# Optimization experiments

Hardware: AMD Instinct MI355X
Metric: run time of the kernel (lower is better)

Reference implementation:

```python
import jax, jax.numpy as jnp
import numpy as np

N_HEADS = 8
NUM_CLASSES = 8
ATTN_INTENSE = 1.0


def setup_inputs() -> dict:
    key = jax.random.key(0)
    k1, k2, k3, k4 = jax.random.split(key, 4)
    bs, width, T = 8, 1536, 1024
    qkv = jax.random.normal(k1, (bs, width, T), dtype=jnp.float32)
    attn_mask = jax.random.randint(k2, (bs, 32, 32), 0, NUM_CLASSES, dtype=jnp.int32)
    # class embedding table: NUM_CLASSES rows + 1 null row (used for the global pass)
    embed_table = jax.random.normal(k3, (NUM_CLASSES + 1, 512), dtype=jnp.float32) * 0.02
    # Conv1d(embed_dim=512 -> 3*ch=192, kernel=1, bias=False) weight
    W_cls = jax.random.normal(k4, (192, 512), dtype=jnp.float32) * 0.02
    return {"qkv": qkv, "attn_mask": attn_mask, "embed_table": embed_table, "W_cls": W_cls}


def _attend(q, k, v, scale):
    # q,k,v: [B, T, C]; returns [B, T, C]
    logits = jnp.einsum('btc,bsc->bts', q * scale, k * scale)
    w = jax.nn.softmax(logits, axis=-1)
    return jnp.einsum('bts,bsc->btc', w, v)


def reference(qkv, attn_mask, embed_table, W_cls):
    bs, width, T = qkv.shape
    H = N_HEADS
    ch = width // (3 * H)            # 64
    scale = ch ** -0.25              # 1/sqrt(sqrt(ch))
    bH = bs * H

    qkv_h = qkv.reshape(bH, 3 * ch, T)
    q = jnp.transpose(qkv_h[:, 0 * ch:1 * ch], (0, 2, 1))  # [bH, T, ch]
    k = jnp.transpose(qkv_h[:, 1 * ch:2 * ch], (0, 2, 1))
    v = jnp.transpose(qkv_h[:, 2 * ch:3 * ch], (0, 2, 1))

    # ---- global pass with null class token ----
    null_tok = W_cls @ embed_table[NUM_CLASSES]  # [3*ch]
    qn, kn, vn = null_tok[:ch], null_tok[ch:2 * ch], null_tok[2 * ch:]
    a = _attend(q + qn, k + kn, v + vn, scale)   # [bH, T, ch]

    # ---- per-region (per segmentation class) attention ----
    seg = attn_mask.reshape(bs, T)
    segs = jnp.repeat(seg, H, axis=0)            # [bH, T], sample-major like qkv reshape

    out = a
    counter = jnp.ones((bH, T), dtype=qkv.dtype)
    for c in range(NUM_CLASSES):
        tok = W_cls @ embed_table[c]             # [3*ch], same token at every region position
        qc, kc, vc = tok[:ch], tok[ch:2 * ch], tok[2 * ch:]
        m = segs == c                            # [bH, T]
        logits = jnp.einsum('btc,bsc->bts', (q + qc) * scale, (k + kc) * scale)
        logits = jnp.where(m[:, None, :], logits, -1e9)   # restrict keys to region
        w = jax.nn.softmax(logits, axis=-1)
        a_c = jnp.einsum('bts,bsc->btc', w, v + vc)
        out = out + jnp.where(m[:, :, None], a_c, 0.0)    # scatter-add onto region queries
        counter = counter + ATTN_INTENSE * m.astype(counter.dtype)

    out = out / counter[:, :, None]              # [bH, T, ch]
    # faithful to original: outs are [ch, T] each, torch.stack(dim=1) -> [ch, bH, T], then reshape
    stacked = jnp.transpose(out, (2, 0, 1))      # [ch, bH, T]
    return stacked.reshape(bs, H * ch, T)
```

## Files before the change

### kernel.cpp

```cpp
#include <hip/hip_runtime.h>
#include <stdint.h>

typedef unsigned short u16;
typedef unsigned int   u32;
typedef __bf16 bf16_t;
typedef bf16_t bf16x8 __attribute__((ext_vector_type(8)));
typedef bf16_t bf16x2 __attribute__((ext_vector_type(2)));
typedef float  f32x2  __attribute__((ext_vector_type(2)));
typedef float  f32x4  __attribute__((ext_vector_type(4)));

#define QSCALE 0.18033688011112042f

__device__ __forceinline__ u32 pkbf(float a, float b) {
  f32x2 x = {a, b};
  bf16x2 y = __builtin_convertvector(x, bf16x2);
  union { bf16x2 v; u32 u; } c; c.v = y; return c.u;
}

__device__ __forceinline__ float fexp2(float x) {
#if __has_builtin(__builtin_amdgcn_exp2f)
  return __builtin_amdgcn_exp2f(x);
#else
  float r;
  asm("v_exp_f32 %0, %1\n\ts_nop 0" : "=v"(r) : "v"(x));
  return r;
#endif
}

__device__ __forceinline__ void gload_lds16(const void* g, void* l) {
  __builtin_amdgcn_global_load_lds(
      (const __attribute__((address_space(1))) void*)g,
      (__attribute__((address_space(3))) void*)l, 16, 0, 0);
}

__global__ __launch_bounds__(256)
void prep_kernel(const float* __restrict__ qkv,
                 const float* __restrict__ W, const float* __restrict__ E,
                 float* __restrict__ tok, u16* __restrict__ tiles) {
  const int B = blockIdx.x;
  const int tid = threadIdx.x;
  if (B >= 1024) {
    const int gw = (B - 1024) * 4 + (tid >> 6);
    const int lane = tid & 63;
    if (gw < 1728) {
      const int c = gw / 192, j = gw - c * 192;
      const f32x4* w4 = (const f32x4*)(W + (size_t)j * 512 + lane * 8);
      const f32x4* e4 = (const f32x4*)(E + (size_t)c * 512 + lane * 8);
      float acc = 0.f;
#pragma unroll
      for (int i = 0; i < 2; ++i) {
        f32x4 w = w4[i], e = e4[i];
        acc += w.x * e.x + w.y * e.y + w.z * e.z + w.w * e.w;
      }
#pragma unroll
      for (int off = 32; off; off >>= 1) acc += __shfl_xor(acc, off, 64);
      if (lane == 0) tok[c * 192 + j] = acc;
    }
    return;
  }
  const int bh = B >> 4, kt = B & 15;
  const int s0 = kt * 64;
  const float* qg = qkv + (size_t)bh * 192 * 1024;
  u16* img = tiles + (size_t)B * 8192;
  {
    const int s = tid & 63, g = tid >> 6;
    const float* kb = qg + (size_t)(64 + g * 16) * 1024 + s0 + s;
    float kf[16];
#pragma unroll
    for (int i = 0; i < 16; ++i) kf[i] = kb[(size_t)i * 1024];
    u32 kp[8];
#pragma unroll
    for (int j2 = 0; j2 < 8; ++j2) kp[j2] = pkbf(kf[2 * j2], kf[2 * j2 + 1]);
    const int xr = (s & 7) << 3;
    *(uint4*)&img[s * 64 + ((g * 16)     ^ xr)] = make_uint4(kp[0], kp[1], kp[2], kp[3]);
    *(uint4*)&img[s * 64 + ((g * 16 + 8) ^ xr)] = make_uint4(kp[4], kp[5], kp[6], kp[7]);
  }
  {
    const int g = tid & 15, dg = tid >> 4;
    const int cp = ((g >> 3) & 1) * 32 + (g & 3) * 8 + ((g >> 2) & 1) * 4;
    const float* vb = qg + (size_t)(128 + dg * 4) * 1024 + s0 + g * 4;
#pragma unroll
    for (int i = 0; i < 4; ++i) {
      f32x4 v = *(const f32x4*)(vb + (size_t)i * 1024);
      const int d = dg * 4 + i;
      *(uint2*)&img[4096 + d * 64 + (cp ^ ((d & 7) << 3))] =
          make_uint2(pkbf(v.x, v.y), pkbf(v.z, v.w));
    }
  }
}

__global__ __launch_bounds__(256, 2)
void attn_kernel(const float* __restrict__ qkv, const int* __restrict__ seg,
                 const float* __restrict__ tok, const u16* __restrict__ tiles,
                 float* __restrict__ out) {
  __shared__ __align__(16) u16 smem[16896];

  const int L  = blockIdx.x;
  const int bh = (L & 7) * 8 + ((L >> 3) & 7);
  const int qb = L >> 6;
  const int b  = bh >> 3;
  const int tid = threadIdx.x, wave = tid >> 6, lane = tid & 63;
  const int quad = lane >> 4, l16 = lane & 15;

  const float* qg   = qkv + (size_t)bh * 192 * 1024;
  const int*   segb = seg + b * 1024;
  const u16*   tbh  = tiles + (size_t)bh * (16 * 8192);

  const int q0i = qb * 128 + wave * 32;
  const int tqA = q0i + l16, tqB = tqA + 16;
  const int mycA = segb[tqA], mycB = segb[tqB];
  int sqA[4], sqB[4];
#pragma unroll
  for (int r = 0; r < 4; ++r) {
    sqA[r] = segb[q0i + quad * 4 + r];
    sqB[r] = segb[q0i + 16 + quad * 4 + r];
  }

  const float* tn  = tok + 8 * 192;
  const float* tcA = tok + mycA * 192;
  const float* tcB = tok + mycB * 192;
  union { u32 w[4]; bf16x8 v; } qA0[2], qAb[2], qB0[2], qBb[2];
#pragma unroll
  for (int kc = 0; kc < 2; ++kc)
#pragma unroll
    for (int jj = 0; jj < 4; ++jj) {
      int d = kc * 32 + quad * 8 + jj * 2;
      float a0 = qg[(size_t)d * 1024 + tqA];
      float a1 = qg[(size_t)(d + 1) * 1024 + tqA];
      float b0 = qg[(size_t)d * 1024 + tqB];
      float b1 = qg[(size_t)(d + 1) * 1024 + tqB];
      qA0[kc].w[jj] = pkbf((a0 + tn[d])  * QSCALE, (a1 + tn[d + 1])  * QSCALE);
      qAb[kc].w[jj] = pkbf((a0 + tcA[d]) * QSCALE, (a1 + tcA[d + 1]) * QSCALE);
      qB0[kc].w[jj] = pkbf((b0 + tn[d])  * QSCALE, (b1 + tn[d + 1])  * QSCALE);
      qBb[kc].w[jj] = pkbf((b0 + tcB[d]) * QSCALE, (b1 + tcB[d + 1]) * QSCALE);
    }

  f32x4 OA0[4], OAb[4], OB0[4], OBb[4];
#pragma unroll
  for (int dt = 0; dt < 4; ++dt) {
    OA0[dt] = (f32x4){0.f, 0.f, 0.f, 0.f};  OAb[dt] = (f32x4){0.f, 0.f, 0.f, 0.f};
    OB0[dt] = (f32x4){0.f, 0.f, 0.f, 0.f};  OBb[dt] = (f32x4){0.f, 0.f, 0.f, 0.f};
  }
  float rsA0 = 0.f, rsAb = 0.f, rsB0 = 0.f, rsBb = 0.f;

  {
    const char* src = (const char*)tbh + tid * 16;
    char* dst = (char*)smem + tid * 16;
#pragma unroll
    for (int i = 0; i < 4; ++i) gload_lds16(src + i * 4096, dst + i * 4096);
  }

  const int xq = (l16 & 7) << 3;

#pragma unroll 2
  for (int kt = 0; kt < 16; ++kt) {
    const int s0 = kt * 64;
    __syncthreads();
    if (kt + 1 < 16) {
      const char* src = (const char*)tbh + (size_t)(kt + 1) * 16384 + tid * 16;
      char* dst = (char*)smem + ((kt + 1) & 1) * 16384 + tid * 16;
#pragma unroll
      for (int i = 0; i < 4; ++i) gload_lds16(src + i * 4096, dst + i * 4096);
    }
    int sk[4][4];
#pragma unroll
    for (int n4 = 0; n4 < 4; ++n4) {
      int4 s4 = *(const int4*)&segb[s0 + n4 * 16 + quad * 4];
      sk[n4][0] = s4.x; sk[n4][1] = s4.y; sk[n4][2] = s4.z; sk[n4][3] = s4.w;
    }

    const u16* ktr = smem + (kt & 1) * 8192;
    const u16* vls = ktr + 4096;

    f32x4 SA0[4], SAb[4], SB0[4], SBb[4];
#pragma unroll
    for (int n4 = 0; n4 < 4; ++n4) {
      const int srow = n4 * 16 + l16;
      f32x4 a0 = {0.f, 0.f, 0.f, 0.f}, ab = {0.f, 0.f, 0.f, 0.f};
      f32x4 c0 = {0.f, 0.f, 0.f, 0.f}, cb = {0.f, 0.f, 0.f, 0.f};
#pragma unroll
      for (int kc = 0; kc < 2; ++kc) {
        bf16x8 kfr = *(const bf16x8*)&ktr[srow * 64 + ((kc * 32 + quad * 8) ^ xq)];
        a0 = __builtin_amdgcn_mfma_f32_16x16x32_bf16(kfr, qA0[kc].v, a0, 0, 0, 0);
        ab = __builtin_amdgcn_mfma_f32_16x16x32_bf16(kfr, qAb[kc].v, ab, 0, 0, 0);
        c0 = __builtin_amdgcn_mfma_f32_16x16x32_bf16(kfr, qB0[kc].v, c0, 0, 0, 0);
        cb = __builtin_amdgcn_mfma_f32_16x16x32_bf16(kfr, qBb[kc].v, cb, 0, 0, 0);
      }
      SA0[n4] = a0; SAb[n4] = ab; SB0[n4] = c0; SBb[n4] = cb;
    }

    union { u32 w[4]; bf16x8 v; } paA0[2], paAb[2], paB0[2], paBb[2];
#define SOFTMAX_PACK(S0, Sb, myc, rs0, rsb, pa0, pab)                          \
    {                                                                          \
      float p0[4][4], pb[4][4];                                                \
      _Pragma("unroll")                                                        \
      for (int n4 = 0; n4 < 4; ++n4)                                           \
        _Pragma("unroll")                                                      \
        for (int r = 0; r < 4; ++r) {                                          \
          p0[n4][r] = fexp2(S0[n4][r]);                                        \
          pb[n4][r] = (sk[n4][r] == myc) ? fexp2(Sb[n4][r]) : 0.f;             \
        }                                                                      \
      _Pragma("unroll")                                                        \
      for (int n4 = 0; n4 < 4; ++n4) {                                         \
        rs0 += (p0[n4][0] + p0[n4][1]) + (p0[n4][2] + p0[n4][3]);              \
        rsb += (pb[n4][0] + pb[n4][1]) + (pb[n4][2] + pb[n4][3]);              \
      }                                                                        \
      _Pragma("unroll")                                                        \
      for (int kc = 0; kc < 2; ++kc) {                                         \
        pa0[kc].w[0] = pkbf(p0[2 * kc][0],     p0[2 * kc][1]);                 \
        pa0[kc].w[1] = pkbf(p0[2 * kc][2],     p0[2 * kc][3]);                 \
        pa0[kc].w[2] = pkbf(p0[2 * kc + 1][0], p0[2 * kc + 1][1]);             \
        pa0[kc].w[3] = pkbf(p0[2 * kc + 1][2], p0[2 * kc + 1][3]);             \
        pab[kc].w[0] = pkbf(pb[2 * kc][0],     pb[2 * kc][1]);                 \
        pab[kc].w[1] = pkbf(pb[2 * kc][2],     pb[2 * kc][3]);                 \
        pab[kc].w[2] = pkbf(pb[2 * kc + 1][0], pb[2 * kc + 1][1]);             \
        pab[kc].w[3] = pkbf(pb[2 * kc + 1][2], pb[2 * kc + 1][3]);             \
      }                                                                        \
    }
    SOFTMAX_PACK(SA0, SAb, mycA, rsA0, rsAb, paA0, paAb)
    SOFTMAX_PACK(SB0, SBb, mycB, rsB0, rsBb, paB0, paBb)
#undef SOFTMAX_PACK

#pragma unroll
    for (int kc = 0; kc < 2; ++kc) {
      const int co = (kc * 32 + quad * 8) ^ xq;
#pragma unroll
      for (int dt = 0; dt < 4; ++dt) {
        bf16x8 vfr = *(const bf16x8*)&vls[(dt * 16 + l16) * 64 + co];
        OA0[dt] = __builtin_amdgcn_mfma_f32_16x16x32_bf16(paA0[kc].v, vfr, OA0[dt], 0, 0, 0);
        OAb[dt] = __builtin_amdgcn_mfma_f32_16x16x32_bf16(paAb[kc].v, vfr, OAb[dt], 0, 0, 0);
        OB0[dt] = __builtin_amdgcn_mfma_f32_16x16x32_bf16(paB0[kc].v, vfr, OB0[dt], 0, 0, 0);
        OBb[dt] = __builtin_amdgcn_mfma_f32_16x16x32_bf16(paBb[kc].v, vfr, OBb[dt], 0, 0, 0);
      }
    }
  }

  rsA0 += __shfl_xor(rsA0, 16, 64);  rsA0 += __shfl_xor(rsA0, 32, 64);
  rsAb += __shfl_xor(rsAb, 16, 64);  rsAb += __shfl_xor(rsAb, 32, 64);
  rsB0 += __shfl_xor(rsB0, 16, 64);  rsB0 += __shfl_xor(rsB0, 32, 64);
  rsBb += __shfl_xor(rsBb, 16, 64);  rsBb += __shfl_xor(rsBb, 32, 64);
  float invA0[4], invAb[4], invB0[4], invBb[4];
#pragma unroll
  for (int r = 0; r < 4; ++r) {
    float a0 = __shfl(rsA0, quad * 4 + r, 16);
    float ab = __shfl(rsAb, quad * 4 + r, 16);
    float b0 = __shfl(rsB0, quad * 4 + r, 16);
    float bb = __shfl(rsBb, quad * 4 + r, 16);
    invA0[r] = (a0 > 0.f) ? 1.f / a0 : 0.f;
    invAb[r] = (ab > 0.f) ? 1.f / ab : 0.f;
    invB0[r] = (b0 > 0.f) ? 1.f / b0 : 0.f;
    invBb[r] = (bb > 0.f) ? 1.f / bb : 0.f;
  }

  __syncthreads();
  float* fbuf = (float*)smem;
  const float* tvn = tok + 8 * 192 + 128;
#pragma unroll
  for (int dt = 0; dt < 4; ++dt) {
    const int d = dt * 16 + l16;
    const float bn = tvn[d];
    f32x4 wA, wB;
#pragma unroll
    for (int r = 0; r < 4; ++r) {
      float bcA = tok[sqA[r] * 192 + 128 + d];
      float bcB = tok[sqB[r] * 192 + 128 + d];
      wA[r] = 0.5f * (OA0[dt][r] * invA0[r] + bn + OAb[dt][r] * invAb[r] + bcA);
      wB[r] = 0.5f * (OB0[dt][r] * invB0[r] + bn + OBb[dt][r] * invBb[r] + bcB);
    }
    *(f32x4*)&fbuf[d * 132 + wave * 32 + quad * 4]      = wA;
    *(f32x4*)&fbuf[d * 132 + wave * 32 + 16 + quad * 4] = wB;
  }
  __syncthreads();
  {
    const size_t obase = (size_t)bh * 1024 + qb * 128;
    for (int i = tid; i < 8192; i += 256) {
      int d = i >> 7, t = i & 127;
      out[(size_t)d * 65536 + obase + t] = fbuf[d * 132 + t];
    }
  }
}

extern "C" void kernel_launch(void* const* d_in, const int* in_sizes, int n_in,
                              void* d_out, int out_size, void* d_ws, size_t ws_size,
                              hipStream_t stream) {
  (void)in_sizes; (void)n_in; (void)out_size; (void)ws_size;
  const float* qkv   = (const float*)d_in[0];
  const int*   amask = (const int*)d_in[1];
  const float* emb   = (const float*)d_in[2];
  const float* wcls  = (const float*)d_in[3];
  float* tok   = (float*)d_ws;
  u16*   tiles = (u16*)((char*)d_ws + 8192);
  float* out = (float*)d_out;

  hipLaunchKernelGGL(prep_kernel, dim3(1456), dim3(256), 0, stream,
                     qkv, wcls, emb, tok, tiles);
  hipLaunchKernelGGL(attn_kernel, dim3(512), dim3(256), 0, stream,
                     qkv, amask, tok, tiles, out);
}
```

Before: 134.2 us.

## Factor class-token logit bias into per-key weights to halve QK MFMAs

```diff
diff --git a/kernel.cpp b/kernel.cpp
--- a/kernel.cpp
+++ b/kernel.cpp
@@ -33,33 +33,30 @@
       (__attribute__((address_space(3))) void*)l, 16, 0, 0);
 }
 
+__global__ void tok_kernel(const float* __restrict__ W, const float* __restrict__ E,
+                           float* __restrict__ tok) {
+  int c = blockIdx.x;
+  int j = threadIdx.x;
+  const f32x4* wr = (const f32x4*)(W + j * 512);
+  const f32x4* er = (const f32x4*)(E + c * 512);
+  float acc = 0.f;
+  for (int i = 0; i < 128; ++i) {
+    f32x4 w = wr[i], e = er[i];
+    acc += w.x * e.x + w.y * e.y + w.z * e.z + w.w * e.w;
+  }
+  tok[c * 192 + j] = acc;
+}
+
 __global__ __launch_bounds__(256)
-void prep_kernel(const float* __restrict__ qkv,
-                 const float* __restrict__ W, const float* __restrict__ E,
-                 float* __restrict__ tok, u16* __restrict__ tiles) {
+void prep_kernel(const float* __restrict__ qkv, const int* __restrict__ seg,
+                 const float* __restrict__ tok, u16* __restrict__ tiles,
+                 float* __restrict__ wtab) {
+  __shared__ float part[256];
   const int B = blockIdx.x;
   const int tid = threadIdx.x;
-  if (B >= 1024) {
-    const int gw = (B - 1024) * 4 + (tid >> 6);
-    const int lane = tid & 63;
-    if (gw < 1728) {
-      const int c = gw / 192, j = gw - c * 192;
-      const f32x4* w4 = (const f32x4*)(W + (size_t)j * 512 + lane * 8);
-      const f32x4* e4 = (const f32x4*)(E + (size_t)c * 512 + lane * 8);
-      float acc = 0.f;
-#pragma unroll
-      for (int i = 0; i < 2; ++i) {
-        f32x4 w = w4[i], e = e4[i];
-        acc += w.x * e.x + w.y * e.y + w.z * e.z + w.w * e.w;
-      }
-#pragma unroll
-      for (int off = 32; off; off >>= 1) acc += __shfl_xor(acc, off, 64);
-      if (lane == 0) tok[c * 192 + j] = acc;
-    }
-    return;
-  }
   const int bh = B >> 4, kt = B & 15;
   const int s0 = kt * 64;
+  const int b  = bh >> 3;
   const float* qg = qkv + (size_t)bh * 192 * 1024;
   u16* img = tiles + (size_t)B * 8192;
   {
@@ -74,6 +71,17 @@
     const int xr = (s & 7) << 3;
     *(uint4*)&img[s * 64 + ((g * 16)     ^ xr)] = make_uint4(kp[0], kp[1], kp[2], kp[3]);
     *(uint4*)&img[s * 64 + ((g * 16 + 8) ^ xr)] = make_uint4(kp[4], kp[5], kp[6], kp[7]);
+    const int cs = seg[b * 1024 + s0 + s];
+    const f32x4* tc = (const f32x4*)(tok + cs * 192 + g * 16);
+    const f32x4* tn = (const f32x4*)(tok + 8 * 192 + g * 16);
+    float pd = 0.f;
+#pragma unroll
+    for (int i = 0; i < 4; ++i) {
+      f32x4 a = tc[i], n = tn[i];
+      pd += (a.x - n.x) * kf[4 * i + 0] + (a.y - n.y) * kf[4 * i + 1] +
+            (a.z - n.z) * kf[4 * i + 2] + (a.w - n.w) * kf[4 * i + 3];
+    }
+    part[s * 4 + g] = pd;
   }
   {
     const int g = tid & 15, dg = tid >> 4;
@@ -87,12 +95,17 @@
           make_uint2(pkbf(v.x, v.y), pkbf(v.z, v.w));
     }
   }
+  __syncthreads();
+  if (tid < 64) {
+    f32x4 p4 = *(const f32x4*)&part[tid * 4];
+    wtab[(size_t)B * 64 + tid] = fexp2(QSCALE * ((p4.x + p4.y) + (p4.z + p4.w)));
+  }
 }
 
 __global__ __launch_bounds__(256, 2)
 void attn_kernel(const float* __restrict__ qkv, const int* __restrict__ seg,
                  const float* __restrict__ tok, const u16* __restrict__ tiles,
-                 float* __restrict__ out) {
+                 const float* __restrict__ wtab, float* __restrict__ out) {
   __shared__ __align__(16) u16 smem[16896];
 
   const int L  = blockIdx.x;
@@ -105,6 +118,7 @@
   const float* qg   = qkv + (size_t)bh * 192 * 1024;
   const int*   segb = seg + b * 1024;
   const u16*   tbh  = tiles + (size_t)bh * (16 * 8192);
+  const float* wbh  = wtab + (size_t)bh * (16 * 64);
 
   const int q0i = qb * 128 + wave * 32;
   const int tqA = q0i + l16, tqB = tqA + 16;
@@ -116,10 +130,8 @@
     sqB[r] = segb[q0i + 16 + quad * 4 + r];
   }
 
-  const float* tn  = tok + 8 * 192;
-  const float* tcA = tok + mycA * 192;
-  const float* tcB = tok + mycB * 192;
-  union { u32 w[4]; bf16x8 v; } qA0[2], qAb[2], qB0[2], qBb[2];
+  const float* tn = tok + 8 * 192;
+  union { u32 w[4]; bf16x8 v; } qA0[2], qB0[2];
 #pragma unroll
   for (int kc = 0; kc < 2; ++kc)
 #pragma unroll
@@ -129,10 +141,8 @@
       float a1 = qg[(size_t)(d + 1) * 1024 + tqA];
       float b0 = qg[(size_t)d * 1024 + tqB];
       float b1 = qg[(size_t)(d + 1) * 1024 + tqB];
-      qA0[kc].w[jj] = pkbf((a0 + tn[d])  * QSCALE, (a1 + tn[d + 1])  * QSCALE);
-      qAb[kc].w[jj] = pkbf((a0 + tcA[d]) * QSCALE, (a1 + tcA[d + 1]) * QSCALE);
-      qB0[kc].w[jj] = pkbf((b0 + tn[d])  * QSCALE, (b1 + tn[d + 1])  * QSCALE);
-      qBb[kc].w[jj] = pkbf((b0 + tcB[d]) * QSCALE, (b1 + tcB[d + 1]) * QSCALE);
+      qA0[kc].w[jj] = pkbf((a0 + tn[d]) * QSCALE, (a1 + tn[d + 1]) * QSCALE);
+      qB0[kc].w[jj] = pkbf((b0 + tn[d]) * QSCALE, (b1 + tn[d + 1]) * QSCALE);
     }
 
   f32x4 OA0[4], OAb[4], OB0[4], OBb[4];
@@ -162,6 +172,10 @@
 #pragma unroll
       for (int i = 0; i < 4; ++i) gload_lds16(src + i * 4096, dst + i * 4096);
     }
+    f32x4 w4[4];
+#pragma unroll
+    for (int n4 = 0; n4 < 4; ++n4)
+      w4[n4] = *(const f32x4*)&wbh[kt * 64 + n4 * 16 + quad * 4];
     int sk[4][4];
 #pragma unroll
     for (int n4 = 0; n4 < 4; ++n4) {
@@ -172,33 +186,32 @@
     const u16* ktr = smem + (kt & 1) * 8192;
     const u16* vls = ktr + 4096;
 
-    f32x4 SA0[4], SAb[4], SB0[4], SBb[4];
+    f32x4 SA[4], SB[4];
+    __builtin_amdgcn_s_setprio(1);
 #pragma unroll
     for (int n4 = 0; n4 < 4; ++n4) {
       const int srow = n4 * 16 + l16;
-      f32x4 a0 = {0.f, 0.f, 0.f, 0.f}, ab = {0.f, 0.f, 0.f, 0.f};
-      f32x4 c0 = {0.f, 0.f, 0.f, 0.f}, cb = {0.f, 0.f, 0.f, 0.f};
+      f32x4 a0 = {0.f, 0.f, 0.f, 0.f}, c0 = {0.f, 0.f, 0.f, 0.f};
 #pragma unroll
       for (int kc = 0; kc < 2; ++kc) {
         bf16x8 kfr = *(const bf16x8*)&ktr[srow * 64 + ((kc * 32 + quad * 8) ^ xq)];
         a0 = __builtin_amdgcn_mfma_f32_16x16x32_bf16(kfr, qA0[kc].v, a0, 0, 0, 0);
-        ab = __builtin_amdgcn_mfma_f32_16x16x32_bf16(kfr, qAb[kc].v, ab, 0, 0, 0);
         c0 = __builtin_amdgcn_mfma_f32_16x16x32_bf16(kfr, qB0[kc].v, c0, 0, 0, 0);
-        cb = __builtin_amdgcn_mfma_f32_16x16x32_bf16(kfr, qBb[kc].v, cb, 0, 0, 0);
       }
-      SA0[n4] = a0; SAb[n4] = ab; SB0[n4] = c0; SBb[n4] = cb;
-    }
+      SA[n4] = a0; SB[n4] = c0;
+    }
+    __builtin_amdgcn_s_setprio(0);
 
     union { u32 w[4]; bf16x8 v; } paA0[2], paAb[2], paB0[2], paBb[2];
-#define SOFTMAX_PACK(S0, Sb, myc, rs0, rsb, pa0, pab)                          \
+#define SOFTMAX_PACK(S, myc, rs0, rsb, pa0, pab)                               \
     {                                                                          \
       float p0[4][4], pb[4][4];                                                \
       _Pragma("unroll")                                                        \
       for (int n4 = 0; n4 < 4; ++n4)                                           \
         _Pragma("unroll")                                                      \
         for (int r = 0; r < 4; ++r) {                                          \
-          p0[n4][r] = fexp2(S0[n4][r]);                                        \
-          pb[n4][r] = (sk[n4][r] == myc) ? fexp2(Sb[n4][r]) : 0.f;             \
+          p0[n4][r] = fexp2(S[n4][r]);                                         \
+          pb[n4][r] = (sk[n4][r] == myc) ? p0[n4][r] * w4[n4][r] : 0.f;        \
         }                                                                      \
       _Pragma("unroll")                                                        \
       for (int n4 = 0; n4 < 4; ++n4) {                                         \
@@ -217,10 +230,11 @@
         pab[kc].w[3] = pkbf(pb[2 * kc + 1][2], pb[2 * kc + 1][3]);             \
       }                                                                        \
     }
-    SOFTMAX_PACK(SA0, SAb, mycA, rsA0, rsAb, paA0, paAb)
-    SOFTMAX_PACK(SB0, SBb, mycB, rsB0, rsBb, paB0, paBb)
+    SOFTMAX_PACK(SA, mycA, rsA0, rsAb, paA0, paAb)
+    SOFTMAX_PACK(SB, mycB, rsB0, rsBb, paB0, paBb)
 #undef SOFTMAX_PACK
 
+    __builtin_amdgcn_s_setprio(1);
 #pragma unroll
     for (int kc = 0; kc < 2; ++kc) {
       const int co = (kc * 32 + quad * 8) ^ xq;
@@ -233,6 +247,7 @@
         OBb[dt] = __builtin_amdgcn_mfma_f32_16x16x32_bf16(paBb[kc].v, vfr, OBb[dt], 0, 0, 0);
       }
     }
+    __builtin_amdgcn_s_setprio(0);
   }
 
   rsA0 += __shfl_xor(rsA0, 16, 64);  rsA0 += __shfl_xor(rsA0, 32, 64);
@@ -290,10 +305,12 @@
   const float* wcls  = (const float*)d_in[3];
   float* tok   = (float*)d_ws;
   u16*   tiles = (u16*)((char*)d_ws + 8192);
+  float* wtab  = (float*)((char*)d_ws + 8192 + 16 * 1024 * 1024);
   float* out = (float*)d_out;
 
-  hipLaunchKernelGGL(prep_kernel, dim3(1456), dim3(256), 0, stream,
-                     qkv, wcls, emb, tok, tiles);
+  hipLaunchKernelGGL(tok_kernel, dim3(9), dim3(192), 0, stream, wcls, emb, tok);
+  hipLaunchKernelGGL(prep_kernel, dim3(1024), dim3(256), 0, stream,
+                     qkv, amask, tok, tiles, wtab);
   hipLaunchKernelGGL(attn_kernel, dim3(512), dim3(256), 0, stream,
-                     qkv, amask, tok, tiles, out);
-}
+                     qkv, amask, tok, tiles, wtab, out);
+}
```

New measurement: 146.5 us. 9.2% more time.
